# Optimization experiments

Measured on AMD Instinct MI355X. Metric: run time of the kernel, lower is better.

Reference implementation:

```python
import jax, jax.numpy as jnp
import numpy as np

D_MODEL = 128
NUM_HEAD = 4
HEAD_DIM = D_MODEL // NUM_HEAD
VOCAB = 32000
MAX_LEN = 4096


def _positional_encoding(max_len, d_model):
    i = jnp.arange(d_model // 2, dtype=jnp.float32)
    pos = jnp.arange(max_len, dtype=jnp.float32)[:, None]
    angle = pos / 10000.0 ** (2.0 * i / d_model)  # [max_len, d_model/2]
    pe = jnp.zeros((max_len, d_model), dtype=jnp.float32)
    pe = pe.at[:, ::2].set(jnp.sin(angle))
    pe = pe.at[:, 1::2].set(jnp.cos(angle))
    return pe  # [max_len, d_model]


def setup_inputs() -> dict:
    key = jax.random.key(0)
    k0, k1, k2, k3, k4, k5 = jax.random.split(key, 6)
    B, S = 2, 4096
    scale = 1.0 / np.sqrt(D_MODEL)
    return {
        "input_seq": jax.random.randint(k0, (B, S), 0, VOCAB, dtype=jnp.int32),
        "embedding": jax.random.normal(k1, (VOCAB, D_MODEL), dtype=jnp.float32),
        "w_q": jax.random.normal(k2, (D_MODEL, D_MODEL), dtype=jnp.float32) * scale,
        "w_k": jax.random.normal(k3, (D_MODEL, D_MODEL), dtype=jnp.float32) * scale,
        "w_v": jax.random.normal(k4, (D_MODEL, D_MODEL), dtype=jnp.float32) * scale,
        "w_o": jax.random.normal(k5, (D_MODEL, D_MODEL), dtype=jnp.float32) * scale,
    }


def reference(input_seq, embedding, w_q, w_k, w_v, w_o):
    B, S = input_seq.shape
    x = embedding[input_seq]  # [B, S, D]
    pe = _positional_encoding(MAX_LEN, D_MODEL)[:S]  # [S, D]
    x = x + pe[None, :, :]
    # torch Linear (no bias): y = x @ W.T
    q = jnp.einsum('bsd,ed->bse', x, w_q)
    k = jnp.einsum('bsd,ed->bse', x, w_k)
    v = jnp.einsum('bsd,ed->bse', x, w_v)
    # faithful to original: plain view (no transpose) splitting into heads
    q = q.reshape(B, NUM_HEAD, S, HEAD_DIM)
    k = k.reshape(B, NUM_HEAD, S, HEAD_DIM)
    v = v.reshape(B, NUM_HEAD, S, HEAD_DIM)
    raw = jnp.einsum('bhqd,bhkd->bhqk', q, k) / np.sqrt(HEAD_DIM)
    # custom abs * tril(-inf) masking
    tril = jnp.tril(jnp.ones((S, S), dtype=raw.dtype))
    masked = jnp.where(tril == 0, -jnp.inf, 1.0).astype(raw.dtype)
    raw = jnp.abs(raw) * masked
    attn = jax.nn.softmax(raw, axis=-1)
    out = jnp.einsum('bhqk,bhkd->bhqd', attn, v)
    out = out.reshape(B, S, D_MODEL)  # faithful plain view
    return jnp.einsum('bsd,ed->bse', out, w_o)
```

## Files before the change

kernel.cpp:

```cpp
#include <hip/hip_runtime.h>
#include <hip/hip_bf16.h>
#include <cmath>

#define D_MODEL 128
#define NUM_HEAD 4
#define HEAD_DIM 32
#define SEQ 4096
#define BATCH 2
#define RROWS 8
#define QROWS 16

typedef __attribute__((ext_vector_type(8))) short short8;
typedef __attribute__((ext_vector_type(4))) float f32x4;

__device__ __forceinline__ float tof(float x) { return x; }
__device__ __forceinline__ float tof(__hip_bfloat16 x) { return __bfloat162float(x); }
__device__ __forceinline__ void storef(float* p, size_t i, float v) { p[i] = v; }
__device__ __forceinline__ void storef(__hip_bfloat16* p, size_t i, float v) { p[i] = __float2bfloat16(v); }

__device__ __forceinline__ void split_bf16(float x, unsigned short& hi, unsigned short& lo)
{
    const unsigned u = __float_as_uint(x);
    const unsigned r = u + 0x7FFFu + ((u >> 16) & 1u);
    hi = (unsigned short)(r >> 16);
    const float hf = __uint_as_float((unsigned)hi << 16);
    const float lf = x - hf;
    const unsigned ul = __float_as_uint(lf);
    const unsigned rl = ul + 0x7FFFu + ((ul >> 16) & 1u);
    lo = (unsigned short)(rl >> 16);
}
__device__ __forceinline__ unsigned short rne_bf16(float x)
{
    const unsigned u = __float_as_uint(x);
    return (unsigned short)((u + 0x7FFFu + ((u >> 16) & 1u)) >> 16);
}

__device__ __forceinline__ void g2l16(const void* g, void* l)
{
    __builtin_amdgcn_global_load_lds(
        (const __attribute__((address_space(1))) void*)g,
        (__attribute__((address_space(3))) void*)l, 16, 0, 0);
}

__global__ __launch_bounds__(256) void prep_kernel(
    const void* wq, const void* wk, const void* wv, const void* wo,
    float* __restrict__ wt4, float* __restrict__ pe, int* __restrict__ flagp)
{
    const int bx  = blockIdx.x;
    const int tid = threadIdx.x;
    __shared__ int sflag;

    if (bx < 64) {
        {
            int weird = 0;
            if (tid < 64) {
                const unsigned short* w16 = (const unsigned short*)wq;
#pragma unroll
                for (int j = 0; j < 4; ++j) {
                    const unsigned short v = w16[(tid * 4 + j) * 2 + 1];
                    const float x = __uint_as_float((unsigned)v << 16);
                    const float a = fabsf(x);
                    if (a > 1e20f || (a > 0.f && a < 1e-20f)) weird++;
                }
#pragma unroll
                for (int off = 32; off; off >>= 1) weird += __shfl_xor(weird, off);
                if (tid == 0) sflag = (weird < 32) ? 1 : 0;
            }
            __syncthreads();
        }
        const int flag = sflag;
        if (bx == 0 && tid == 0) *flagp = flag;

        const int m = bx >> 4;
        const void* w = (m == 0) ? wq : (m == 1) ? wk : (m == 2) ? wv : wo;
        const int item = (bx & 15) * 256 + tid;
        const int e  = item & 127;
        const int dq = item >> 7;
        float4 v;
        if (flag) {
            v = *(const float4*)((const float*)w + (size_t)e * 128 + dq * 4);
        } else {
            const __hip_bfloat16* wb = (const __hip_bfloat16*)w + (size_t)e * 128 + dq * 4;
            v = make_float4(tof(wb[0]), tof(wb[1]), tof(wb[2]), tof(wb[3]));
        }
        *(float4*)&wt4[(((size_t)m * 32 + dq) * 128 + e) * 4] = v;
    } else {
        const int item = (bx - 64) * 256 + tid;
        const int s = item >> 6;
        const int i = item & 63;
        const double inv = 1.0 / pow(10000.0, (double)i / 64.0);
        const double a = (double)s * inv;
        float2 sc;
        sc.x = (float)sin(a);
        sc.y = (float)cos(a);
        *(float2*)&pe[(size_t)s * 128 + i * 2] = sc;
    }
}

template <typename T>
__device__ __forceinline__ void qkv_body(
    const int* __restrict__ seq, const T* __restrict__ emb,
    const float* __restrict__ wt4, const float* __restrict__ pe,
    unsigned short* __restrict__ Qhi, unsigned short* __restrict__ Qlo,
    unsigned short* __restrict__ Khi, unsigned short* __restrict__ Klo,
    unsigned short* __restrict__ Vthi, unsigned short* __restrict__ Vtlo)
{
    const int tid = threadIdx.x;
    const int e   = tid & 127;
    const int grp = tid >> 7;
    const int r0  = blockIdx.x * QROWS;

    __shared__ __align__(16) float xs[QROWS][D_MODEL];
    __shared__ __align__(16) unsigned short vsh[2][QROWS][D_MODEL];

#pragma unroll
    for (int k = 0; k < 4; ++k) {
        const int idx = k * 512 + tid;
        const int r  = idx >> 7;
        const int ee = idx & 127;
        const int srow = r0 + r;
        xs[r][ee] = tof(emb[(size_t)seq[srow] * D_MODEL + ee])
                  + pe[(size_t)(srow & (SEQ - 1)) * D_MODEL + ee];
    }
    __syncthreads();

    float aq[4], ak[4], av[4];
#pragma unroll
    for (int r = 0; r < 4; ++r) { aq[r] = 0.f; ak[r] = 0.f; av[r] = 0.f; }

    const int rbase = grp * 4;
    const float4* wq4 = (const float4*)wt4;
    const float4* wk4 = wq4 + 4096;
    const float4* wv4 = wq4 + 8192;

    for (int dq = 0; dq < 32; ++dq) {
        float4 xr[4];
#pragma unroll
        for (int r = 0; r < 4; ++r) xr[r] = *(const float4*)&xs[rbase + r][dq * 4];
        const float4 wq_ = wq4[dq * 128 + e];
        const float4 wk_ = wk4[dq * 128 + e];
        const float4 wv_ = wv4[dq * 128 + e];
#pragma unroll
        for (int r = 0; r < 4; ++r) {
            aq[r] += xr[r].x * wq_.x; aq[r] += xr[r].y * wq_.y;
            aq[r] += xr[r].z * wq_.z; aq[r] += xr[r].w * wq_.w;
            ak[r] += xr[r].x * wk_.x; ak[r] += xr[r].y * wk_.y;
            ak[r] += xr[r].z * wk_.z; ak[r] += xr[r].w * wk_.w;
            av[r] += xr[r].x * wv_.x; av[r] += xr[r].y * wv_.y;
            av[r] += xr[r].z * wv_.z; av[r] += xr[r].w * wv_.w;
        }
    }

    const float scale = 0.17677669529663687f;
#pragma unroll
    for (int r = 0; r < 4; ++r) {
        const int row = rbase + r;
        const size_t o = (size_t)(r0 + row) * D_MODEL + e;
        unsigned short hi, lo;
        split_bf16(aq[r] * scale, hi, lo); Qhi[o] = hi; Qlo[o] = lo;
        split_bf16(ak[r], hi, lo);         Khi[o] = hi; Klo[o] = lo;
        split_bf16(av[r], hi, lo);         vsh[0][row][e] = hi; vsh[1][row][e] = lo;
    }
    __syncthreads();

    {
        const int b  = r0 >> 12;
        const int s0 = r0 & (SEQ - 1);
        const int h  = s0 >> 10;
        const size_t vtb = (size_t)(b * 4 + h) * (32 * SEQ);
        const int hl = tid >> 8;
        const int d  = (tid >> 3) & 31;
        const int j  = tid & 7;
        short8 tmp;
#pragma unroll
        for (int i = 0; i < 8; ++i) {
            const int kl = j * 8 + i;
            tmp[i] = (short)vsh[hl][kl >> 2][(kl & 3) * 32 + d];
        }
        unsigned short* dst = (hl ? Vtlo : Vthi) + vtb + (size_t)d * SEQ
                            + (size_t)(s0 & 1023) * 4 + j * 8;
        *(short8*)dst = tmp;
    }
}

__global__ __launch_bounds__(512, 4) void qkv_kernel(
    const int* __restrict__ seq, const void* emb,
    const float* __restrict__ wt4, const float* __restrict__ pe,
    unsigned short* Qhi, unsigned short* Qlo,
    unsigned short* Khi, unsigned short* Klo,
    unsigned short* Vthi, unsigned short* Vtlo,
    const int* __restrict__ flag)
{
    if (*flag)
        qkv_body<float>(seq, (const float*)emb, wt4, pe,
                        Qhi, Qlo, Khi, Klo, Vthi, Vtlo);
    else
        qkv_body<__hip_bfloat16>(seq, (const __hip_bfloat16*)emb, wt4, pe,
                                 Qhi, Qlo, Khi, Klo, Vthi, Vtlo);
}

__global__ __launch_bounds__(256, 6) void attn_kernel(
    const unsigned short* __restrict__ Qhi, const unsigned short* __restrict__ Qlo,
    const unsigned short* __restrict__ Khi, const unsigned short* __restrict__ Klo,
    const unsigned short* __restrict__ Vthi, const unsigned short* __restrict__ Vtlo,
    float* __restrict__ Apart, float* __restrict__ lbuf)
{
    const int bh   = blockIdx.x;
    const int by   = blockIdx.y;
    const int kh   = blockIdx.z;
    const int qt   = (by < 32) ? by : 95 - by;
    const size_t baseQ  = (size_t)(bh >> 2) * SEQ * D_MODEL + (size_t)(bh & 3) * SEQ * HEAD_DIM;
    const size_t baseVt = (size_t)bh * (32 * SEQ);

    const int tid  = threadIdx.x;
    const int wid  = __builtin_amdgcn_readfirstlane(tid >> 6);
    const int lane = tid & 63;
    const int rt   = wid;
    const int quad = lane >> 4;
    const int col  = lane & 15;

    __shared__ float shbuf[4 * 544];
    __shared__ __align__(16) unsigned char kv[2][8192];
    float* pb = &shbuf[wid * 544];

    const int qrow0 = qt * 64 + rt * 16;

    short8 qhiF, qloF;
    {
        const size_t qo = baseQ + (size_t)(qrow0 + col) * HEAD_DIM + quad * 8;
        qhiF = *(const short8*)(Qhi + qo);
        qloF = *(const short8*)(Qlo + qo);
    }

    f32x4 O0 = {0.f, 0.f, 0.f, 0.f};
    f32x4 O1 = {0.f, 0.f, 0.f, 0.f};
    float l[4] = {0.f, 0.f, 0.f, 0.f};

    const int N   = 2 * (qt + 1);
    const int nb  = N >> 2, rem = N & 3;
    const int cnt  = nb + ((kh < rem) ? 1 : 0);
    const int cbeg = kh * nb + ((kh < rem) ? kh : rem);
    const int cend = cbeg + cnt;

    const int r4 = lane >> 2, s0 = lane & 3;
    auto stage = [&](int bufi, int kbase) {
#pragma unroll
        for (int half = 0; half < 2; ++half) {
            const int row = half * 16 + r4;
            const int seg = s0 ^ (row & 3);
            const unsigned short* src;
            if (wid == 0)      src = Khi  + baseQ  + (size_t)(kbase + row) * HEAD_DIM + seg * 8;
            else if (wid == 1) src = Klo  + baseQ  + (size_t)(kbase + row) * HEAD_DIM + seg * 8;
            else if (wid == 2) src = Vthi + baseVt + (size_t)row * SEQ + kbase + seg * 8;
            else               src = Vtlo + baseVt + (size_t)row * SEQ + kbase + seg * 8;
            g2l16(src, &kv[bufi][wid * 2048 + half * 1024]);
        }
    };
    auto frag = [&](int bufi, int plane, int row) -> short8 {
        const int byte = plane * 2048 + row * 64 + ((quad ^ (row & 3)) << 4);
        return *(const short8*)(&kv[bufi][byte]);
    };

    if (cnt > 0) {
        stage(0, cbeg * 32);
        int p = 0;
        for (int c = cbeg; c < cend; ++c) {
            const int kbase = c * 32;
            const bool pre = (c + 1 < cend);
            if (pre) {
                stage(p ^ 1, (c + 1) * 32);
                asm volatile("s_waitcnt vmcnt(2)" ::: "memory");
            } else {
                asm volatile("s_waitcnt vmcnt(0)" ::: "memory");
            }
            __builtin_amdgcn_s_barrier();

            const short8 k0h = frag(p, 0, col);
            const short8 k0l = frag(p, 1, col);
            const short8 k1h = frag(p, 0, col + 16);
            const short8 k1l = frag(p, 1, col + 16);

            f32x4 s0v = {0.f, 0.f, 0.f, 0.f};
            f32x4 s1v = {0.f, 0.f, 0.f, 0.f};
            s0v = __builtin_amdgcn_mfma_f32_16x16x32_bf16(qhiF, k0h, s0v, 0, 0, 0);
            s0v = __builtin_amdgcn_mfma_f32_16x16x32_bf16(qhiF, k0l, s0v, 0, 0, 0);
            s0v = __builtin_amdgcn_mfma_f32_16x16x32_bf16(qloF, k0h, s0v, 0, 0, 0);
            s1v = __builtin_amdgcn_mfma_f32_16x16x32_bf16(qhiF, k1h, s1v, 0, 0, 0);
            s1v = __builtin_amdgcn_mfma_f32_16x16x32_bf16(qhiF, k1l, s1v, 0, 0, 0);
            s1v = __builtin_amdgcn_mfma_f32_16x16x32_bf16(qloF, k1h, s1v, 0, 0, 0);

#pragma unroll
            for (int r = 0; r < 4; ++r) {
                const int rowg = qrow0 + quad * 4 + r;
                const float e0 = (kbase + col      <= rowg) ? __expf(fabsf(s0v[r])) : 0.f;
                const float e1 = (kbase + 16 + col <= rowg) ? __expf(fabsf(s1v[r])) : 0.f;
                l[r] += e0 + e1;
                pb[(quad * 4 + r) * 34 + col]      = e0;
                pb[(quad * 4 + r) * 34 + 16 + col] = e1;
            }
            short8 ph;
            {
                const float* pr = &pb[col * 34 + quad * 8];
#pragma unroll
                for (int j = 0; j < 8; ++j) ph[j] = (short)rne_bf16(pr[j]);
            }

            const short8 v0h = frag(p, 2, col);
            const short8 v0l = frag(p, 3, col);
            const short8 v1h = frag(p, 2, col + 16);
            const short8 v1l = frag(p, 3, col + 16);

            O0 = __builtin_amdgcn_mfma_f32_16x16x32_bf16(ph, v0h, O0, 0, 0, 0);
            O0 = __builtin_amdgcn_mfma_f32_16x16x32_bf16(ph, v0l, O0, 0, 0, 0);
            O1 = __builtin_amdgcn_mfma_f32_16x16x32_bf16(ph, v1h, O1, 0, 0, 0);
            O1 = __builtin_amdgcn_mfma_f32_16x16x32_bf16(ph, v1l, O1, 0, 0, 0);

            __builtin_amdgcn_s_barrier();
            p ^= 1;
        }
    }

#pragma unroll
    for (int off = 1; off < 16; off <<= 1) {
#pragma unroll
        for (int r = 0; r < 4; ++r) l[r] += __shfl_xor(l[r], off, 64);
    }

    float* Ap = Apart + (size_t)kh * (BATCH * SEQ * D_MODEL) + baseQ;
#pragma unroll
    for (int r = 0; r < 4; ++r) {
        const int row = qrow0 + quad * 4 + r;
        Ap[(size_t)row * HEAD_DIM + col]      = O0[r];
        Ap[(size_t)row * HEAD_DIM + 16 + col] = O1[r];
    }
    if (col == 0) {
        float* lp = lbuf + ((size_t)kh * (BATCH * NUM_HEAD) + bh) * SEQ;
#pragma unroll
        for (int r = 0; r < 4; ++r)
            lp[qrow0 + quad * 4 + r] = l[r];
    }
}

template <typename T>
__device__ __forceinline__ void out_proj_body(
    const float* __restrict__ Apart, const float* __restrict__ lbuf,
    const float* __restrict__ wo4t, T* __restrict__ out)
{
    const int tid = threadIdx.x;
    const int e   = tid & 127;
    const int grp = tid >> 7;
    const int r0  = blockIdx.x * RROWS;

    __shared__ __align__(16) float xs[RROWS][D_MODEL];
#pragma unroll
    for (int k = 0; k < 4; ++k) {
        const int idx = k * 256 + tid;
        const int rr = idx >> 7;
        const int ee = idx & 127;
        const int gr = r0 + rr;
        const int b  = gr >> 12;
        const int s  = gr & (SEQ - 1);
        const int bh = b * 4 + (s >> 10);
        const int hr = ((s & 1023) << 2) + (ee >> 5);
        const size_t ai = (size_t)gr * D_MODEL + ee;
        float sum = 0.f, Ls = 0.f;
#pragma unroll
        for (int kh = 0; kh < 4; ++kh) {
            sum += Apart[(size_t)kh * (BATCH * SEQ * D_MODEL) + ai];
            Ls  += lbuf[((size_t)kh * (BATCH * NUM_HEAD) + bh) * SEQ + hr];
        }
        xs[rr][ee] = sum * (1.f / Ls);
    }
    __syncthreads();

    float acc[4] = {0.f, 0.f, 0.f, 0.f};
    const int rbase = grp * 4;
    const float4* w4 = (const float4*)wo4t;

    for (int dq = 0; dq < 32; ++dq) {
        float4 xr[4];
#pragma unroll
        for (int r = 0; r < 4; ++r) xr[r] = *(const float4*)&xs[rbase + r][dq * 4];
        const float4 w_ = w4[dq * 128 + e];
#pragma unroll
        for (int r = 0; r < 4; ++r) {
            acc[r] += xr[r].x * w_.x; acc[r] += xr[r].y * w_.y;
            acc[r] += xr[r].z * w_.z; acc[r] += xr[r].w * w_.w;
        }
    }
#pragma unroll
    for (int r = 0; r < 4; ++r)
        storef(out, (size_t)(r0 + rbase + r) * D_MODEL + e, acc[r]);
}

__global__ __launch_bounds__(256, 4) void out_proj_kernel(
    const float* __restrict__ Apart, const float* __restrict__ lbuf,
    const float* __restrict__ wo4t, void* out,
    const int* __restrict__ flag)
{
    if (*flag)
        out_proj_body<float>(Apart, lbuf, wo4t, (float*)out);
    else
        out_proj_body<__hip_bfloat16>(Apart, lbuf, wo4t, (__hip_bfloat16*)out);
}

extern "C" void kernel_launch(void* const* d_in, const int* in_sizes, int n_in,
                              void* d_out, int out_size, void* d_ws, size_t ws_size,
                              hipStream_t stream) {
    const int* seq = (const int*)d_in[0];
    const void* emb = d_in[1];
    const void* wq  = d_in[2];
    const void* wk  = d_in[3];
    const void* wv  = d_in[4];
    const void* wo  = d_in[5];

    const size_t N = (size_t)BATCH * SEQ * D_MODEL;
    int*            flag = (int*)d_ws;
    unsigned short* Qhi  = (unsigned short*)((char*)d_ws + 256);
    unsigned short* Qlo  = Qhi + N;
    unsigned short* Khi  = Qlo + N;
    unsigned short* Klo  = Khi + N;
    unsigned short* Vthi = Klo + N;
    unsigned short* Vtlo = Vthi + N;
    float*          Apart = (float*)(Vtlo + N);
    float*          lbuf  = Apart + 4 * N;
    float*          wt4   = lbuf + 4 * BATCH * NUM_HEAD * SEQ;
    float*          pe    = wt4 + 65536;

    prep_kernel<<<dim3(64 + 1024), dim3(256), 0, stream>>>(wq, wk, wv, wo, wt4, pe, flag);
    qkv_kernel<<<dim3(BATCH * SEQ / QROWS), dim3(512), 0, stream>>>(
        seq, emb, wt4, pe,
        Qhi, Qlo, Khi, Klo, Vthi, Vtlo, flag);
    attn_kernel<<<dim3(BATCH * NUM_HEAD, 64, 4), dim3(256), 0, stream>>>(
        Qhi, Qlo, Khi, Klo, Vthi, Vtlo, Apart, lbuf);
    out_proj_kernel<<<dim3(BATCH * SEQ / RROWS), dim3(256), 0, stream>>>(
        Apart, lbuf, wt4 + 49152, d_out, flag);
}
```

Measured before the change: 158.5 us.

## Triple-buffer attention K/V staging and compute positional encoding by angle recurrence

The attention loop moves from double to triple buffering of K/V tiles in shared memory. Loads are issued two chunks ahead and one of the two barriers per iteration is removed. The probability scratch stride is padded to 36 so it can be read back with float4 loads, and launch bounds drop to 4 blocks per SIMD to fit the larger LDS footprint. The positional-encoding prep replaces per-element double sin/cos with a rotation recurrence over 128 positions per thread, cutting the prep grid from 1088 to 72 blocks, at the cost of serial work per thread and possible accumulated rounding error.

```diff
diff --git a/kernel.cpp b/kernel.cpp
--- a/kernel.cpp
+++ b/kernel.cpp
@@ -85,15 +85,24 @@
         }
         *(float4*)&wt4[(((size_t)m * 32 + dq) * 128 + e) * 4] = v;
     } else {
-        const int item = (bx - 64) * 256 + tid;
-        const int s = item >> 6;
-        const int i = item & 63;
+        const int idx   = (bx - 64) * 256 + tid;
+        const int i     = idx & 63;
+        const int chunk = idx >> 6;
+        const int s0    = chunk * 128;
         const double inv = 1.0 / pow(10000.0, (double)i / 64.0);
-        const double a = (double)s * inv;
-        float2 sc;
-        sc.x = (float)sin(a);
-        sc.y = (float)cos(a);
-        *(float2*)&pe[(size_t)s * 128 + i * 2] = sc;
+        const double a0  = (double)s0 * inv;
+        double c  = cos(a0), s = sin(a0);
+        const double cd = cos(inv), sd = sin(inv);
+        float2* row = (float2*)&pe[(size_t)s0 * 128 + i * 2];
+        for (int k = 0; k < 128; ++k) {
+            float2 sc;
+            sc.x = (float)s;
+            sc.y = (float)c;
+            row[(size_t)k * 64] = sc;
+            const double cn = c * cd - s * sd;
+            s = s * cd + c * sd;
+            c = cn;
+        }
     }
 }
 
@@ -199,7 +208,7 @@
                                  Qhi, Qlo, Khi, Klo, Vthi, Vtlo);
 }
 
-__global__ __launch_bounds__(256, 6) void attn_kernel(
+__global__ __launch_bounds__(256, 4) void attn_kernel(
     const unsigned short* __restrict__ Qhi, const unsigned short* __restrict__ Qlo,
     const unsigned short* __restrict__ Khi, const unsigned short* __restrict__ Klo,
     const unsigned short* __restrict__ Vthi, const unsigned short* __restrict__ Vtlo,
@@ -219,9 +228,9 @@
     const int quad = lane >> 4;
     const int col  = lane & 15;
 
-    __shared__ float shbuf[4 * 544];
-    __shared__ __align__(16) unsigned char kv[2][8192];
-    float* pb = &shbuf[wid * 544];
+    __shared__ float shbuf[4 * 576];
+    __shared__ __align__(16) unsigned char kv[3][8192];
+    float* pb = &shbuf[wid * 576];
 
     const int qrow0 = qt * 64 + rt * 16;
 
@@ -240,14 +249,13 @@
     const int nb  = N >> 2, rem = N & 3;
     const int cnt  = nb + ((kh < rem) ? 1 : 0);
     const int cbeg = kh * nb + ((kh < rem) ? kh : rem);
-    const int cend = cbeg + cnt;
-
-    const int r4 = lane >> 2, s0 = lane & 3;
+
+    const int r4 = lane >> 2, sseg = lane & 3;
     auto stage = [&](int bufi, int kbase) {
 #pragma unroll
         for (int half = 0; half < 2; ++half) {
             const int row = half * 16 + r4;
-            const int seg = s0 ^ (row & 3);
+            const int seg = sseg ^ (row & 3);
             const unsigned short* src;
             if (wid == 0)      src = Khi  + baseQ  + (size_t)(kbase + row) * HEAD_DIM + seg * 8;
             else if (wid == 1) src = Klo  + baseQ  + (size_t)(kbase + row) * HEAD_DIM + seg * 8;
@@ -263,22 +271,24 @@
 
     if (cnt > 0) {
         stage(0, cbeg * 32);
-        int p = 0;
-        for (int c = cbeg; c < cend; ++c) {
+        if (cnt > 1) stage(1, (cbeg + 1) * 32);
+        int cur = 0;
+        for (int i = 0; i < cnt; ++i) {
+            const int c = cbeg + i;
             const int kbase = c * 32;
-            const bool pre = (c + 1 < cend);
-            if (pre) {
-                stage(p ^ 1, (c + 1) * 32);
-                asm volatile("s_waitcnt vmcnt(2)" ::: "memory");
-            } else {
-                asm volatile("s_waitcnt vmcnt(0)" ::: "memory");
+            if (i + 1 < cnt) { asm volatile("s_waitcnt vmcnt(2)" ::: "memory"); }
+            else             { asm volatile("s_waitcnt vmcnt(0)" ::: "memory"); }
+            __builtin_amdgcn_s_barrier();
+            __builtin_amdgcn_sched_barrier(0);
+            if (i + 2 < cnt) {
+                int nx = cur + 2; if (nx > 2) nx -= 3;
+                stage(nx, (c + 2) * 32);
             }
-            __builtin_amdgcn_s_barrier();
-
-            const short8 k0h = frag(p, 0, col);
-            const short8 k0l = frag(p, 1, col);
-            const short8 k1h = frag(p, 0, col + 16);
-            const short8 k1l = frag(p, 1, col + 16);
+
+            const short8 k0h = frag(cur, 0, col);
+            const short8 k0l = frag(cur, 1, col);
+            const short8 k1h = frag(cur, 0, col + 16);
+            const short8 k1l = frag(cur, 1, col + 16);
 
             f32x4 s0v = {0.f, 0.f, 0.f, 0.f};
             f32x4 s1v = {0.f, 0.f, 0.f, 0.f};
@@ -295,28 +305,30 @@
                 const float e0 = (kbase + col      <= rowg) ? __expf(fabsf(s0v[r])) : 0.f;
                 const float e1 = (kbase + 16 + col <= rowg) ? __expf(fabsf(s1v[r])) : 0.f;
                 l[r] += e0 + e1;
-                pb[(quad * 4 + r) * 34 + col]      = e0;
-                pb[(quad * 4 + r) * 34 + 16 + col] = e1;
+                pb[(quad * 4 + r) * 36 + col]      = e0;
+                pb[(quad * 4 + r) * 36 + 16 + col] = e1;
             }
             short8 ph;
             {
-                const float* pr = &pb[col * 34 + quad * 8];
-#pragma unroll
-                for (int j = 0; j < 8; ++j) ph[j] = (short)rne_bf16(pr[j]);
+                const float4 p01 = *(const float4*)&pb[col * 36 + quad * 8];
+                const float4 p23 = *(const float4*)&pb[col * 36 + quad * 8 + 4];
+                ph[0] = (short)rne_bf16(p01.x); ph[1] = (short)rne_bf16(p01.y);
+                ph[2] = (short)rne_bf16(p01.z); ph[3] = (short)rne_bf16(p01.w);
+                ph[4] = (short)rne_bf16(p23.x); ph[5] = (short)rne_bf16(p23.y);
+                ph[6] = (short)rne_bf16(p23.z); ph[7] = (short)rne_bf16(p23.w);
             }
 
-            const short8 v0h = frag(p, 2, col);
-            const short8 v0l = frag(p, 3, col);
-            const short8 v1h = frag(p, 2, col + 16);
-            const short8 v1l = frag(p, 3, col + 16);
+            const short8 v0h = frag(cur, 2, col);
+            const short8 v0l = frag(cur, 3, col);
+            const short8 v1h = frag(cur, 2, col + 16);
+            const short8 v1l = frag(cur, 3, col + 16);
 
             O0 = __builtin_amdgcn_mfma_f32_16x16x32_bf16(ph, v0h, O0, 0, 0, 0);
             O0 = __builtin_amdgcn_mfma_f32_16x16x32_bf16(ph, v0l, O0, 0, 0, 0);
             O1 = __builtin_amdgcn_mfma_f32_16x16x32_bf16(ph, v1h, O1, 0, 0, 0);
             O1 = __builtin_amdgcn_mfma_f32_16x16x32_bf16(ph, v1l, O1, 0, 0, 0);
 
-            __builtin_amdgcn_s_barrier();
-            p ^= 1;
+            cur = (cur == 2) ? 0 : cur + 1;
         }
     }
 
@@ -427,7 +439,7 @@
     float*          wt4   = lbuf + 4 * BATCH * NUM_HEAD * SEQ;
     float*          pe    = wt4 + 65536;
 
-    prep_kernel<<<dim3(64 + 1024), dim3(256), 0, stream>>>(wq, wk, wv, wo, wt4, pe, flag);
+    prep_kernel<<<dim3(64 + 8), dim3(256), 0, stream>>>(wq, wk, wv, wo, wt4, pe, flag);
     qkv_kernel<<<dim3(BATCH * SEQ / QROWS), dim3(512), 0, stream>>>(
         seq, emb, wt4, pe,
         Qhi, Qlo, Khi, Klo, Vthi, Vtlo, flag);
```

Result: no change. 160.2 us (+1.1%).
